# Performance work log

Measured on AMD Instinct MI355X. Metric: run time of the kernel, lower is better.

## Reference

```python
import jax, jax.numpy as jnp
import numpy as np

B, NNEG, D, E = 16384, 10, 8, 64
N_ENT = 500000  # sum(domain_dims.values())
N_PAIRS = D * (D - 1) // 2


def setup_inputs() -> dict:
    key = jax.random.key(0)
    k1, k2, k3, k4, k5 = jax.random.split(key, 5)
    return {
        "pos_x": jax.random.randint(k1, (B, D), 0, N_ENT, dtype=jnp.int32),
        "neg_x": jax.random.randint(k2, (B, NNEG, D), 0, N_ENT, dtype=jnp.int32),
        "emb_table": jax.random.normal(k3, (N_ENT, E), dtype=jnp.float32) * 0.01,
        "pair_w": jax.random.uniform(k4, (N_PAIRS,), dtype=jnp.float32),
        "c": jax.random.uniform(k5, (1,), dtype=jnp.float32),
    }


def _obtain_score(x, emb_table, pair_w, c):
    # x: [..., D] int indices into the shared embedding table
    e = emb_table[x]                                   # [..., D, E] gather
    gram = jnp.einsum('...de,...fe->...df', e, e)      # [..., D, D] pairwise dots
    iu, ju = np.triu_indices(D, k=1)
    pair_dots = gram[..., iu, ju]                      # [..., N_PAIRS]
    # NOTE: the original torch code never increments k inside obtain_score,
    # so EVERY pair is scaled by exp(pair_W['0']). We replicate that faithfully.
    r = pair_dots * jnp.exp(pair_w[0])
    return jnp.exp(jnp.sum(r, axis=-1) + c[0])         # [...]


def reference(pos_x, neg_x, emb_table, pair_w, c):
    pos_score = _obtain_score(pos_x, emb_table, pair_w, c)   # [B]
    # vectorized over the negative-sample axis (original loops in Python)
    neg_score = _obtain_score(neg_x, emb_table, pair_w, c)   # [B, NNEG]
    return pos_score, neg_score
```

## Files before the change

kernel.cpp:

```cpp
#include <hip/hip_runtime.h>

constexpr int B     = 16384;
constexpr int NNEG  = 10;
constexpr int D     = 8;
constexpr int E     = 64;
constexpr int ROWS  = B * (1 + NNEG);
constexpr int RPW   = 8;

__global__ __launch_bounds__(256) void APE_61555471286335_kernel(
    const int*   __restrict__ pos_x,
    const int*   __restrict__ neg_x,
    const float* __restrict__ emb,
    const float* __restrict__ pair_w,
    const float* __restrict__ c,
    float*       __restrict__ out)
{
    const int tid  = blockIdx.x * blockDim.x + threadIdx.x;
    const int wave = tid >> 6;
    const int lane = threadIdx.x & 63;
    const int g    = lane >> 3;
    const int t    = lane & 7;
    const int row  = wave * RPW + g;

    const int* idx = (row < B) ? (pos_x + (size_t)row * D)
                               : (neg_x + (size_t)(row - B) * D);
    const int4 i0 = *(const int4*)(idx);
    const int4 i1 = *(const int4*)(idx + 4);
    const int ids[D] = {i0.x, i0.y, i0.z, i0.w, i1.x, i1.y, i1.z, i1.w};

    float4 s0 = make_float4(0.f, 0.f, 0.f, 0.f), s1 = s0;
    float4 q0 = s0, q1 = s0;
#pragma unroll
    for (int d = 0; d < D; ++d) {
        const float* r = emb + (size_t)ids[d] * E + t * 8;
        const float4 v0 = *(const float4*)(r);
        const float4 v1 = *(const float4*)(r + 4);
        s0.x += v0.x; s0.y += v0.y; s0.z += v0.z; s0.w += v0.w;
        s1.x += v1.x; s1.y += v1.y; s1.z += v1.z; s1.w += v1.w;
        q0.x += v0.x * v0.x; q0.y += v0.y * v0.y;
        q0.z += v0.z * v0.z; q0.w += v0.w * v0.w;
        q1.x += v1.x * v1.x; q1.y += v1.y * v1.y;
        q1.z += v1.z * v1.z; q1.w += v1.w * v1.w;
    }

    float a = s0.x * s0.x + s0.y * s0.y + s0.z * s0.z + s0.w * s0.w
            + s1.x * s1.x + s1.y * s1.y + s1.z * s1.z + s1.w * s1.w;
    float q = q0.x + q0.y + q0.z + q0.w + q1.x + q1.y + q1.z + q1.w;

#pragma unroll
    for (int off = 4; off > 0; off >>= 1) {
        a += __shfl_xor(a, off, 64);
        q += __shfl_xor(q, off, 64);
    }

    if (t == 0) {
        const float pair_sum = 0.5f * (a - q);
        out[row] = expf(pair_sum * expf(pair_w[0]) + c[0]);
    }
}

extern "C" void kernel_launch(void* const* d_in, const int* in_sizes, int n_in,
                              void* d_out, int out_size, void* d_ws, size_t ws_size,
                              hipStream_t stream) {
    const int*   pos_x  = (const int*)  d_in[0];
    const int*   neg_x  = (const int*)  d_in[1];
    const float* emb    = (const float*)d_in[2];
    const float* pair_w = (const float*)d_in[3];
    const float* c      = (const float*)d_in[4];
    float*       out    = (float*)      d_out;

    constexpr int BLOCK = 256;
    constexpr int ROWS_PER_BLOCK = (BLOCK / 64) * RPW;
    static_assert(ROWS % ROWS_PER_BLOCK == 0, "exact grid");
    const int grid = ROWS / ROWS_PER_BLOCK;

    APE_61555471286335_kernel<<<grid, BLOCK, 0, stream>>>(
        pos_x, neg_x, emb, pair_w, c, out);
}
```

Baseline: 240.3 us.

## Gather embedding rows via direct global-to-LDS loads with 16 lanes per row

Embedding rows are now fetched with global_load_lds (16-byte async DMA straight into LDS) instead of register float4 loads. Each wave now handles 4 rows with 16 lanes per row, and each lane moves one 16-byte chunk per table row. The kernel waits on vmcnt and a block barrier, then reads the chunks back from LDS. The reduction is merged into one value, (sum)^2 - sumsq, before the shuffles. This adds a 32KB LDS footprint per block, an LDS round-trip and a barrier, and halves the rows per wave, so it doubles the grid size.

```diff
diff --git a/kernel.cpp b/kernel.cpp
--- a/kernel.cpp
+++ b/kernel.cpp
@@ -1,11 +1,21 @@
 #include <hip/hip_runtime.h>
+#include <cstdint>
 
 constexpr int B     = 16384;
 constexpr int NNEG  = 10;
 constexpr int D     = 8;
 constexpr int E     = 64;
 constexpr int ROWS  = B * (1 + NNEG);
-constexpr int RPW   = 8;
+constexpr int RPW   = 4;
+constexpr int WPB   = 4;
+constexpr int LDS_PER_WAVE = D * 1024;
+
+__device__ __forceinline__ void dma16(const float* gp, void* lp) {
+    __builtin_amdgcn_global_load_lds(
+        (const __attribute__((address_space(1))) void*)gp,
+        (__attribute__((address_space(3))) void*)lp,
+        16, 0, 0);
+}
 
 __global__ __launch_bounds__(256) void APE_61555471286335_kernel(
     const int*   __restrict__ pos_x,
@@ -15,47 +25,49 @@
     const float* __restrict__ c,
     float*       __restrict__ out)
 {
-    const int tid  = blockIdx.x * blockDim.x + threadIdx.x;
-    const int wave = tid >> 6;
+    __shared__ char smem[WPB * LDS_PER_WAVE];
+
     const int lane = threadIdx.x & 63;
-    const int g    = lane >> 3;
-    const int t    = lane & 7;
+    const int wid  = threadIdx.x >> 6;
+    const int wave = blockIdx.x * WPB + wid;
+    const int g    = lane >> 4;
+    const int t    = lane & 15;
     const int row  = wave * RPW + g;
+
+    char* base = smem + wid * LDS_PER_WAVE;
 
     const int* idx = (row < B) ? (pos_x + (size_t)row * D)
                                : (neg_x + (size_t)(row - B) * D);
     const int4 i0 = *(const int4*)(idx);
     const int4 i1 = *(const int4*)(idx + 4);
-    const int ids[D] = {i0.x, i0.y, i0.z, i0.w, i1.x, i1.y, i1.z, i1.w};
+    const int id[D] = {i0.x, i0.y, i0.z, i0.w, i1.x, i1.y, i1.z, i1.w};
 
-    float4 s0 = make_float4(0.f, 0.f, 0.f, 0.f), s1 = s0;
-    float4 q0 = s0, q1 = s0;
 #pragma unroll
     for (int d = 0; d < D; ++d) {
-        const float* r = emb + (size_t)ids[d] * E + t * 8;
-        const float4 v0 = *(const float4*)(r);
-        const float4 v1 = *(const float4*)(r + 4);
-        s0.x += v0.x; s0.y += v0.y; s0.z += v0.z; s0.w += v0.w;
-        s1.x += v1.x; s1.y += v1.y; s1.z += v1.z; s1.w += v1.w;
-        q0.x += v0.x * v0.x; q0.y += v0.y * v0.y;
-        q0.z += v0.z * v0.z; q0.w += v0.w * v0.w;
-        q1.x += v1.x * v1.x; q1.y += v1.y * v1.y;
-        q1.z += v1.z * v1.z; q1.w += v1.w * v1.w;
+        const float* gp = emb + (size_t)id[d] * E + t * 4;
+        dma16(gp, base + d * 1024 + lane * 16);
     }
 
-    float a = s0.x * s0.x + s0.y * s0.y + s0.z * s0.z + s0.w * s0.w
-            + s1.x * s1.x + s1.y * s1.y + s1.z * s1.z + s1.w * s1.w;
-    float q = q0.x + q0.y + q0.z + q0.w + q1.x + q1.y + q1.z + q1.w;
+    __builtin_amdgcn_s_waitcnt(0x0f70);
+    __syncthreads();
+
+    float4 s = make_float4(0.f, 0.f, 0.f, 0.f), q = s;
+#pragma unroll
+    for (int d = 0; d < D; ++d) {
+        const float4 v = *(const float4*)(base + d * 1024 + lane * 16);
+        s.x += v.x; s.y += v.y; s.z += v.z; s.w += v.w;
+        q.x += v.x * v.x; q.y += v.y * v.y;
+        q.z += v.z * v.z; q.w += v.w * v.w;
+    }
+    float p = s.x * s.x + s.y * s.y + s.z * s.z + s.w * s.w
+            - (q.x + q.y + q.z + q.w);
 
 #pragma unroll
-    for (int off = 4; off > 0; off >>= 1) {
-        a += __shfl_xor(a, off, 64);
-        q += __shfl_xor(q, off, 64);
-    }
+    for (int off = 8; off > 0; off >>= 1)
+        p += __shfl_xor(p, off, 64);
 
     if (t == 0) {
-        const float pair_sum = 0.5f * (a - q);
-        out[row] = expf(pair_sum * expf(pair_w[0]) + c[0]);
+        out[row] = expf(0.5f * p * expf(pair_w[0]) + c[0]);
     }
 }
 
@@ -70,7 +82,7 @@
     float*       out    = (float*)      d_out;
 
     constexpr int BLOCK = 256;
-    constexpr int ROWS_PER_BLOCK = (BLOCK / 64) * RPW;
+    constexpr int ROWS_PER_BLOCK = WPB * RPW;
     static_assert(ROWS % ROWS_PER_BLOCK == 0, "exact grid");
     const int grid = ROWS / ROWS_PER_BLOCK;
 
```

After: 211.0 us. 12.2% less time.
